# Optimization experiments

Measured on AMD Instinct MI355X. Metric: run time of the kernel, lower is better.

## Reference

```python
import jax, jax.numpy as jnp
import numpy as np

B, L = 2048, 128          # (src,tgt) pairs x walk positions
K = 4                     # num_layers + 1
ENC = 108                 # enc_dim
D2, D3, D4 = 172, 512, 172
NKEYS = 1_000_000         # unique (batch,node,time,sign) keys in nodetime2emb_maps


def setup_inputs() -> dict:
    key = jax.random.key(0)
    ks = jax.random.split(key, 8)
    emb_table = jax.random.uniform(ks[0], (NKEYS, 2, K), dtype=jnp.float32)
    idx = jax.random.randint(ks[1], (B, L), 0, NKEYS, dtype=jnp.int32)
    W1 = jax.random.normal(ks[2], (K, ENC), dtype=jnp.float32) * (1.0 / np.sqrt(K))
    b1 = jnp.zeros((ENC,), dtype=jnp.float32)
    W2 = jax.random.normal(ks[3], (ENC, ENC), dtype=jnp.float32) * (1.0 / np.sqrt(ENC))
    b2 = jnp.zeros((ENC,), dtype=jnp.float32)
    x2 = jax.random.normal(ks[4], (B, L, D2), dtype=jnp.float32)
    fc1_w = jax.random.normal(ks[5], (ENC + D2, D3), dtype=jnp.float32) * (1.0 / np.sqrt(ENC + D2))
    fc1_b = jnp.zeros((D3,), dtype=jnp.float32)
    fc2_w = jax.random.normal(ks[6], (D3, D4), dtype=jnp.float32) * (1.0 / np.sqrt(D3))
    fc2_b = jnp.zeros((D4,), dtype=jnp.float32)
    return {"emb_table": emb_table, "idx": idx, "W1": W1, "b1": b1, "W2": W2,
            "b2": b2, "x2": x2, "fc1_w": fc1_w, "fc1_b": fc1_b,
            "fc2_w": fc2_w, "fc2_b": fc2_b}


def reference(emb_table, idx, W1, b1, W2, b2, x2, fc1_w, fc1_b, fc2_w, fc2_b):
    # --- PositionEncoder.forward: gather per-(node,time) encodings [B,L,2,K]
    enc = emb_table[idx]
    # --- get_trainable_encodings: Linear(K->ENC), ReLU, Linear(ENC->ENC), sum over src/tgt axis
    h = jax.nn.relu(jnp.einsum('blsk,ke->blse', enc, W1) + b1)
    h = jnp.einsum('blse,ef->blsf', h, W2) + b2
    pe = h.sum(axis=-2)                      # [B, L, ENC]
    # --- MergeLayer (edge_embedding_type='concat'): concat + fc1 + ReLU + fc2
    x = jnp.concatenate([pe, x2], axis=-1)   # [B, L, ENC + D2]
    z = jax.nn.relu(x @ fc1_w + fc1_b) @ fc2_w + fc2_b  # [B, L, D4]
    return z
```

## Files before the change

### kernel.cpp

```cpp
#include <hip/hip_runtime.h>
#include <stdint.h>

typedef __bf16 bf16x8 __attribute__((ext_vector_type(8)));
typedef float  f32x4  __attribute__((ext_vector_type(4)));
typedef unsigned short u16x4 __attribute__((ext_vector_type(4)));

#define XROW_B 576
#define HROW_B 1024
#define LDS_SZ 65536
#define WSTG   40960

#define WS_FC1T   0
#define WS_FC2T   294912
#define WS_BIAS   491520

__device__ __forceinline__ unsigned short f2bf(float f) {
  union { float f; unsigned u; } c; c.f = f;
  unsigned u = c.u;
  u += 0x7FFFu + ((u >> 16) & 1u);
  return (unsigned short)(u >> 16);
}

__global__ void POLAR_prep_fc1(const float* __restrict__ W2,
                               const float* __restrict__ fc1_w,
                               const float* __restrict__ fc1_b,
                               const float* __restrict__ b2,
                               unsigned short* __restrict__ fc1t,
                               float* __restrict__ bias_eff) {
  int n = blockIdx.x;
  int k = threadIdx.x;
  float v = 0.f;
  if (k < 108) {
    for (int f = 0; f < 108; ++f) v += W2[k*108 + f] * fc1_w[f*512 + n];
  } else if (k < 280) {
    v = fc1_w[k*512 + n];
  }
  fc1t[n*288 + k] = f2bf(v);
  if (k == 0) {
    float bb = fc1_b[n];
    for (int f = 0; f < 108; ++f) bb += 2.f * b2[f] * fc1_w[f*512 + n];
    bias_eff[n] = bb;
  }
}

__global__ void POLAR_prep_fc2(const float* __restrict__ fc2_w,
                               unsigned short* __restrict__ fc2t) {
  int n = blockIdx.x;
  int k = threadIdx.x;
  float v = (n < 172) ? fc2_w[k*172 + n] : 0.f;
  fc2t[n*512 + k] = f2bf(v);
}

__global__ __launch_bounds__(512, 4) void POLAR_fused(
    const float* __restrict__ emb, const int* __restrict__ idx,
    const float* __restrict__ W1, const float* __restrict__ b1,
    const float* __restrict__ x2,
    const unsigned short* __restrict__ fc1t,
    const float* __restrict__ bias_eff,
    const unsigned short* __restrict__ fc2t,
    const float* __restrict__ fc2b,
    float* __restrict__ out)
{
  __shared__ __attribute__((aligned(16))) char smem[LDS_SZ];
  const int tid  = threadIdx.x;
  const int lane = tid & 63;
  const int w    = tid >> 6;
  const int blk  = blockIdx.x;
  const int l15  = lane & 15;
  const int l4   = lane >> 4;

  const char* fb1 = (const char*)fc1t;
  const char* fb2 = (const char*)fc2t;

  unsigned boff1[4];
  bf16x8 bva[4], bvb[4];
  #pragma unroll
  for (int j = 0; j < 4; ++j) {
    boff1[j] = (unsigned)((w * 64 + j * 16 + l15) * 576 + l4 * 16);
    bva[j] = *(const bf16x8*)(fb1 + boff1[j]);
  }

  const int r  = tid >> 3;
  const int li = tid & 7;
  int key = idx[(size_t)blk * 64 + r];
  const float* ep = emb + (size_t)key * 8;
  f32x4 e0 = *(const f32x4*)ep;
  f32x4 e1 = *(const f32x4*)(ep + 4);

  {
    float* wsl = (float*)(smem + WSTG);
    if (tid < 432) wsl[tid] = W1[tid];
    else if (tid < 540) wsl[tid] = b1[tid - 432];
    int t2 = tid + 512;
    if (t2 < 540) wsl[t2] = b1[t2 - 432];
  }
  __syncthreads();

  {
    const float* Ws = (const float*)(smem + WSTG);
    unsigned sw = ((unsigned)(r >> 1) & 3u) << 4;
    for (int e = li; e < 108; e += 8) {
      float w0 = Ws[e], w1v = Ws[108 + e], w2v = Ws[216 + e], w3v = Ws[324 + e];
      float bb = Ws[432 + e];
      float a0 = fmaxf(e0.x*w0 + e0.y*w1v + e0.z*w2v + e0.w*w3v + bb, 0.f);
      float a1 = fmaxf(e1.x*w0 + e1.y*w1v + e1.z*w2v + e1.w*w3v + bb, 0.f);
      *(unsigned short*)(smem + r * XROW_B + ((unsigned)(2*e) ^ sw)) = f2bf(a0 + a1);
    }
  }

  {
    const f32x4* x2v = (const f32x4*)(x2 + (size_t)blk * 64 * 172);
    #pragma unroll 1
    for (int t = tid; t < 64 * 43; t += 512) {
      int rr = t / 43, c4 = t - rr * 43;
      f32x4 v = x2v[t];
      u16x4 s; s.x = f2bf(v.x); s.y = f2bf(v.y); s.z = f2bf(v.z); s.w = f2bf(v.w);
      unsigned be = 216u + 8u * (unsigned)c4;
      unsigned sw = ((unsigned)(rr >> 1) & 3u) << 4;
      *(u16x4*)(smem + rr * XROW_B + (be ^ sw)) = s;
    }
    if (tid < 64) {
      unsigned sw = ((unsigned)(tid >> 1) & 3u) << 4;
      union { long2 l; } z; z.l.x = 0; z.l.y = 0;
      *(long2*)(smem + tid * XROW_B + (560u ^ sw)) = z.l;
    }
  }
  __syncthreads();

  f32x4 acc[4][4];
  #pragma unroll
  for (int i = 0; i < 4; ++i)
    #pragma unroll
    for (int j = 0; j < 4; ++j)
      acc[i][j] = (f32x4){0.f, 0.f, 0.f, 0.f};

  unsigned abase[4];
  #pragma unroll
  for (int i = 0; i < 4; ++i) {
    int row = i * 16 + l15;
    abase[i] = (unsigned)(row * XROW_B)
             + (((unsigned)(l4 * 16)) ^ ((((unsigned)row >> 1) & 3u) << 4));
  }

  bf16x8 af[4];
  #pragma unroll 1
  for (int kt = 0; kt < 8; kt += 2) {
    #pragma unroll
    for (int j = 0; j < 4; ++j)
      bvb[j] = *(const bf16x8*)(fb1 + boff1[j] + (kt + 1) * 64);
    #pragma unroll
    for (int i = 0; i < 4; ++i)
      af[i] = *(const bf16x8*)(smem + abase[i] + kt * 64);
    #pragma unroll
    for (int i = 0; i < 4; ++i)
      #pragma unroll
      for (int j = 0; j < 4; ++j)
        acc[i][j] = __builtin_amdgcn_mfma_f32_16x16x32_bf16(af[i], bva[j], acc[i][j], 0, 0, 0);
    #pragma unroll
    for (int j = 0; j < 4; ++j)
      bva[j] = *(const bf16x8*)(fb1 + boff1[j] + (kt + 2) * 64);
    #pragma unroll
    for (int i = 0; i < 4; ++i)
      af[i] = *(const bf16x8*)(smem + abase[i] + (kt + 1) * 64);
    #pragma unroll
    for (int i = 0; i < 4; ++i)
      #pragma unroll
      for (int j = 0; j < 4; ++j)
        acc[i][j] = __builtin_amdgcn_mfma_f32_16x16x32_bf16(af[i], bvb[j], acc[i][j], 0, 0, 0);
  }
  {
    #pragma unroll
    for (int i = 0; i < 4; ++i)
      af[i] = *(const bf16x8*)(smem + abase[i] + 8 * 64);
    #pragma unroll
    for (int i = 0; i < 4; ++i)
      #pragma unroll
      for (int j = 0; j < 4; ++j)
        acc[i][j] = __builtin_amdgcn_mfma_f32_16x16x32_bf16(af[i], bva[j], acc[i][j], 0, 0, 0);
  }
  __syncthreads();

  const int wm4 = w >> 2;
  const int wn4 = w & 3;
  unsigned boff2[3];
  bf16x8 b2a[3][2], b2b[3][2];
  #pragma unroll
  for (int j = 0; j < 3; ++j) {
    boff2[j] = (unsigned)((wn4 * 48 + j * 16 + l15) * 1024 + l4 * 16);
    #pragma unroll
    for (int s = 0; s < 2; ++s)
      b2a[j][s] = *(const bf16x8*)(fb2 + boff2[j] + s * 64);
  }

  {
    const int odd = lane & 1;
    #pragma unroll
    for (int i = 0; i < 4; ++i) {
      #pragma unroll
      for (int j = 0; j < 4; ++j) {
        int col0 = w * 64 + j * 16 + l15;
        float be = bias_eff[col0];
        float a0 = fmaxf(acc[i][j][0] + be, 0.f);
        float a1 = fmaxf(acc[i][j][1] + be, 0.f);
        float a2 = fmaxf(acc[i][j][2] + be, 0.f);
        float a3 = fmaxf(acc[i][j][3] + be, 0.f);
        float t0 = odd ? a0 : a2;
        float t1 = odd ? a1 : a3;
        float p0 = __shfl_xor(t0, 1);
        float p1 = __shfl_xor(t1, 1);
        unsigned w0 = odd ? ((unsigned)f2bf(p0) | ((unsigned)f2bf(a2) << 16))
                          : ((unsigned)f2bf(a0) | ((unsigned)f2bf(p0) << 16));
        unsigned w1 = odd ? ((unsigned)f2bf(p1) | ((unsigned)f2bf(a3) << 16))
                          : ((unsigned)f2bf(a1) | ((unsigned)f2bf(p1) << 16));
        int row0 = i * 16 + l4 * 4 + (odd ? 2 : 0);
        int row1 = row0 + 1;
        unsigned cb = (unsigned)((col0 & ~1) * 2);
        *(unsigned*)(smem + row0 * HROW_B + (cb ^ (((unsigned)row0 & 7u) << 4))) = w0;
        *(unsigned*)(smem + row1 * HROW_B + (cb ^ (((unsigned)row1 & 7u) << 4))) = w1;
      }
    }
  }
  __syncthreads();

  f32x4 acc2[2][3];
  #pragma unroll
  for (int i = 0; i < 2; ++i)
    #pragma unroll
    for (int j = 0; j < 3; ++j)
      acc2[i][j] = (f32x4){0.f, 0.f, 0.f, 0.f};

  unsigned h0base[2], swr2[2];
  #pragma unroll
  for (int i = 0; i < 2; ++i) {
    int row = wm4 * 32 + i * 16 + l15;
    h0base[i] = (unsigned)(row * HROW_B);
    swr2[i] = (((unsigned)row & 7u) << 4);
  }

  bf16x8 a2[2][2];
  #pragma unroll 1
  for (int kt = 0; kt < 8; kt += 2) {
    #pragma unroll
    for (int j = 0; j < 3; ++j)
      #pragma unroll
      for (int s = 0; s < 2; ++s)
        b2b[j][s] = *(const bf16x8*)(fb2 + boff2[j] + (kt + 1) * 128 + s * 64);
    #pragma unroll
    for (int i = 0; i < 2; ++i)
      #pragma unroll
      for (int s = 0; s < 2; ++s)
        a2[i][s] = *(const bf16x8*)(smem + h0base[i]
                     + (((unsigned)(kt * 128 + s * 64 + l4 * 16)) ^ swr2[i]));
    #pragma unroll
    for (int s = 0; s < 2; ++s)
      #pragma unroll
      for (int i = 0; i < 2; ++i)
        #pragma unroll
        for (int j = 0; j < 3; ++j)
          acc2[i][j] = __builtin_amdgcn_mfma_f32_16x16x32_bf16(a2[i][s], b2a[j][s], acc2[i][j], 0, 0, 0);
    if (kt < 6) {
      #pragma unroll
      for (int j = 0; j < 3; ++j)
        #pragma unroll
        for (int s = 0; s < 2; ++s)
          b2a[j][s] = *(const bf16x8*)(fb2 + boff2[j] + (kt + 2) * 128 + s * 64);
    }
    #pragma unroll
    for (int i = 0; i < 2; ++i)
      #pragma unroll
      for (int s = 0; s < 2; ++s)
        a2[i][s] = *(const bf16x8*)(smem + h0base[i]
                     + (((unsigned)((kt + 1) * 128 + s * 64 + l4 * 16)) ^ swr2[i]));
    #pragma unroll
    for (int s = 0; s < 2; ++s)
      #pragma unroll
      for (int i = 0; i < 2; ++i)
        #pragma unroll
        for (int j = 0; j < 3; ++j)
          acc2[i][j] = __builtin_amdgcn_mfma_f32_16x16x32_bf16(a2[i][s], b2b[j][s], acc2[i][j], 0, 0, 0);
  }

  const size_t orow0 = (size_t)blk * 64;
  #pragma unroll
  for (int j = 0; j < 3; ++j) {
    int col = wn4 * 48 + j * 16 + l15;
    if (col < 172) {
      float bias = fc2b[col];
      #pragma unroll
      for (int i = 0; i < 2; ++i) {
        #pragma unroll
        for (int r2 = 0; r2 < 4; ++r2) {
          int row = wm4 * 32 + i * 16 + l4 * 4 + r2;
          out[(orow0 + row) * 172 + col] = acc2[i][j][r2] + bias;
        }
      }
    }
  }
}

extern "C" void kernel_launch(void* const* d_in, const int* in_sizes, int n_in,
                              void* d_out, int out_size, void* d_ws, size_t ws_size,
                              hipStream_t stream) {
  (void)in_sizes; (void)n_in; (void)out_size; (void)ws_size;
  const float* emb   = (const float*)d_in[0];
  const int*   idx   = (const int*)d_in[1];
  const float* W1    = (const float*)d_in[2];
  const float* b1    = (const float*)d_in[3];
  const float* W2    = (const float*)d_in[4];
  const float* b2    = (const float*)d_in[5];
  const float* x2    = (const float*)d_in[6];
  const float* fc1_w = (const float*)d_in[7];
  const float* fc1_b = (const float*)d_in[8];
  const float* fc2_w = (const float*)d_in[9];
  const float* fc2_b = (const float*)d_in[10];
  float* out = (float*)d_out;
  char* ws = (char*)d_ws;
  unsigned short* fc1t = (unsigned short*)(ws + WS_FC1T);
  unsigned short* fc2t = (unsigned short*)(ws + WS_FC2T);
  float* bias_eff = (float*)(ws + WS_BIAS);

  POLAR_prep_fc1<<<512, 288, 0, stream>>>(W2, fc1_w, fc1_b, b2, fc1t, bias_eff);
  POLAR_prep_fc2<<<192, 512, 0, stream>>>(fc2_w, fc2t);
  POLAR_fused<<<4096, 512, 0, stream>>>(emb, idx, W1, b1, x2, fc1t, bias_eff,
                                        fc2t, fc2_b, out);
}
```

Measured before the change: 350.2 us.

## Split row preparation into separate kernel and stream bf16 rows via global_load_lds

The gather, first-layer encoding and x2 bf16 conversion move out of the fused GEMM kernel into a new row-prep kernel. It writes swizzled bf16 rows to a workspace buffer, and the GEMM kernel copies them into LDS with global_load_lds DMA. The GEMM kernel's launch bounds change from 4 to 2 blocks per CU. This is meant to take the latency-bound gather and conversion off the MFMA kernel, at the cost of an extra write and read of about 150 MB of bf16 data. The old fused kernel stays as a fallback when the workspace is too small.

```diff
diff --git a/kernel.cpp b/kernel.cpp
--- a/kernel.cpp
+++ b/kernel.cpp
@@ -8,17 +8,24 @@
 #define XROW_B 576
 #define HROW_B 1024
 #define LDS_SZ 65536
-#define WSTG   40960
 
 #define WS_FC1T   0
 #define WS_FC2T   294912
 #define WS_BIAS   491520
+#define WS_XBF    524288
+#define WS_NEED   (524288 + (size_t)262144 * 576)
 
 __device__ __forceinline__ unsigned short f2bf(float f) {
   union { float f; unsigned u; } c; c.f = f;
   unsigned u = c.u;
   u += 0x7FFFu + ((u >> 16) & 1u);
   return (unsigned short)(u >> 16);
+}
+
+__device__ __forceinline__ void g2l16(const void* g, void* l) {
+  __builtin_amdgcn_global_load_lds(
+      (const __attribute__((address_space(1))) void*)g,
+      (__attribute__((address_space(3))) void*)l, 16, 0, 0);
 }
 
 __global__ void POLAR_prep_fc1(const float* __restrict__ W2,
@@ -51,10 +58,63 @@
   fc2t[n*512 + k] = f2bf(v);
 }
 
-__global__ __launch_bounds__(512, 4) void POLAR_fused(
+__global__ __launch_bounds__(256) void POLAR_rows(
     const float* __restrict__ emb, const int* __restrict__ idx,
     const float* __restrict__ W1, const float* __restrict__ b1,
-    const float* __restrict__ x2,
+    const float* __restrict__ x2, unsigned short* __restrict__ xbf)
+{
+  __shared__ float wsl[540];
+  const int tid = threadIdx.x, blk = blockIdx.x;
+
+  const int p = tid >> 1, q = tid & 1;
+  const size_t row = (size_t)blk * 128 + p;
+  int key = idx[row];
+  const float* ep = emb + (size_t)key * 8;
+  f32x4 e0 = *(const f32x4*)ep;
+  f32x4 e1 = *(const f32x4*)(ep + 4);
+
+  for (int t = tid; t < 540; t += 256) wsl[t] = (t < 432) ? W1[t] : b1[t - 432];
+  __syncthreads();
+
+  {
+    char* xrow = (char*)xbf + row * XROW_B;
+    unsigned sw = ((unsigned)(p >> 1) & 3u) << 4;
+    int ebase = q * 54;
+    #pragma unroll 3
+    for (int i = 0; i < 27; ++i) {
+      int e = ebase + 2 * i;
+      float wa0 = wsl[e],     wa1 = wsl[108+e],   wa2 = wsl[216+e],   wa3 = wsl[324+e],   ba = wsl[432+e];
+      float wb0 = wsl[e+1],   wb1 = wsl[109+e],   wb2 = wsl[217+e],   wb3 = wsl[325+e],   bb = wsl[433+e];
+      float a = fmaxf(e0.x*wa0 + e0.y*wa1 + e0.z*wa2 + e0.w*wa3 + ba, 0.f)
+              + fmaxf(e1.x*wa0 + e1.y*wa1 + e1.z*wa2 + e1.w*wa3 + ba, 0.f);
+      float b = fmaxf(e0.x*wb0 + e0.y*wb1 + e0.z*wb2 + e0.w*wb3 + bb, 0.f)
+              + fmaxf(e1.x*wb0 + e1.y*wb1 + e1.z*wb2 + e1.w*wb3 + bb, 0.f);
+      unsigned pk = (unsigned)f2bf(a) | ((unsigned)f2bf(b) << 16);
+      *(unsigned*)(xrow + ((unsigned)(2 * e) ^ sw)) = pk;
+    }
+  }
+
+  {
+    const f32x4* x2v = (const f32x4*)(x2 + (size_t)blk * 128 * 172);
+    char* xbase = (char*)xbf + (size_t)blk * 128 * XROW_B;
+    #pragma unroll 2
+    for (int t = tid; t < 128 * 43; t += 256) {
+      int rr = t / 43, c4 = t - rr * 43;
+      f32x4 v = x2v[t];
+      u16x4 s; s.x = f2bf(v.x); s.y = f2bf(v.y); s.z = f2bf(v.z); s.w = f2bf(v.w);
+      unsigned sw = ((unsigned)(rr >> 1) & 3u) << 4;
+      *(u16x4*)(xbase + rr * XROW_B + ((216u + 8u * (unsigned)c4) ^ sw)) = s;
+    }
+    if (tid < 128) {
+      unsigned sw = ((unsigned)(tid >> 1) & 3u) << 4;
+      union { long2 l; } z; z.l.x = 0; z.l.y = 0;
+      *(long2*)(xbase + tid * XROW_B + (560u ^ sw)) = z.l;
+    }
+  }
+}
+
+__global__ __launch_bounds__(512, 2) void POLAR_gemm(
+    const unsigned short* __restrict__ xbf,
     const unsigned short* __restrict__ fc1t,
     const float* __restrict__ bias_eff,
     const unsigned short* __restrict__ fc2t,
@@ -80,50 +140,11 @@
     bva[j] = *(const bf16x8*)(fb1 + boff1[j]);
   }
 
-  const int r  = tid >> 3;
-  const int li = tid & 7;
-  int key = idx[(size_t)blk * 64 + r];
-  const float* ep = emb + (size_t)key * 8;
-  f32x4 e0 = *(const f32x4*)ep;
-  f32x4 e1 = *(const f32x4*)(ep + 4);
-
-  {
-    float* wsl = (float*)(smem + WSTG);
-    if (tid < 432) wsl[tid] = W1[tid];
-    else if (tid < 540) wsl[tid] = b1[tid - 432];
-    int t2 = tid + 512;
-    if (t2 < 540) wsl[t2] = b1[t2 - 432];
-  }
-  __syncthreads();
-
-  {
-    const float* Ws = (const float*)(smem + WSTG);
-    unsigned sw = ((unsigned)(r >> 1) & 3u) << 4;
-    for (int e = li; e < 108; e += 8) {
-      float w0 = Ws[e], w1v = Ws[108 + e], w2v = Ws[216 + e], w3v = Ws[324 + e];
-      float bb = Ws[432 + e];
-      float a0 = fmaxf(e0.x*w0 + e0.y*w1v + e0.z*w2v + e0.w*w3v + bb, 0.f);
-      float a1 = fmaxf(e1.x*w0 + e1.y*w1v + e1.z*w2v + e1.w*w3v + bb, 0.f);
-      *(unsigned short*)(smem + r * XROW_B + ((unsigned)(2*e) ^ sw)) = f2bf(a0 + a1);
-    }
-  }
-
-  {
-    const f32x4* x2v = (const f32x4*)(x2 + (size_t)blk * 64 * 172);
-    #pragma unroll 1
-    for (int t = tid; t < 64 * 43; t += 512) {
-      int rr = t / 43, c4 = t - rr * 43;
-      f32x4 v = x2v[t];
-      u16x4 s; s.x = f2bf(v.x); s.y = f2bf(v.y); s.z = f2bf(v.z); s.w = f2bf(v.w);
-      unsigned be = 216u + 8u * (unsigned)c4;
-      unsigned sw = ((unsigned)(rr >> 1) & 3u) << 4;
-      *(u16x4*)(smem + rr * XROW_B + (be ^ sw)) = s;
-    }
-    if (tid < 64) {
-      unsigned sw = ((unsigned)(tid >> 1) & 3u) << 4;
-      union { long2 l; } z; z.l.x = 0; z.l.y = 0;
-      *(long2*)(smem + tid * XROW_B + (560u ^ sw)) = z.l;
-    }
+  {
+    const char* xsrc = (const char*)xbf + (size_t)blk * (64 * XROW_B);
+    #pragma unroll
+    for (int c = w; c < 36; c += 8)
+      g2l16(xsrc + c * 1024 + lane * 16, smem + c * 1024);
   }
   __syncthreads();
 
@@ -298,10 +319,256 @@
   }
 }
 
+__global__ __launch_bounds__(512, 4) void POLAR_fused_fb(
+    const float* __restrict__ emb, const int* __restrict__ idx,
+    const float* __restrict__ W1, const float* __restrict__ b1,
+    const float* __restrict__ x2,
+    const unsigned short* __restrict__ fc1t,
+    const float* __restrict__ bias_eff,
+    const unsigned short* __restrict__ fc2t,
+    const float* __restrict__ fc2b,
+    float* __restrict__ out)
+{
+  __shared__ __attribute__((aligned(16))) char smem[LDS_SZ];
+  const int tid  = threadIdx.x;
+  const int lane = tid & 63;
+  const int w    = tid >> 6;
+  const int blk  = blockIdx.x;
+  const int l15  = lane & 15;
+  const int l4   = lane >> 4;
+
+  const char* fb1 = (const char*)fc1t;
+  const char* fb2 = (const char*)fc2t;
+
+  unsigned boff1[4];
+  bf16x8 bva[4], bvb[4];
+  #pragma unroll
+  for (int j = 0; j < 4; ++j) {
+    boff1[j] = (unsigned)((w * 64 + j * 16 + l15) * 576 + l4 * 16);
+    bva[j] = *(const bf16x8*)(fb1 + boff1[j]);
+  }
+
+  const int r  = tid >> 3;
+  const int li = tid & 7;
+  int key = idx[(size_t)blk * 64 + r];
+  const float* ep = emb + (size_t)key * 8;
+  f32x4 e0 = *(const f32x4*)ep;
+  f32x4 e1 = *(const f32x4*)(ep + 4);
+
+  {
+    float* wsl = (float*)(smem + 40960);
+    if (tid < 432) wsl[tid] = W1[tid];
+    else if (tid < 540) wsl[tid] = b1[tid - 432];
+    int t2 = tid + 512;
+    if (t2 < 540) wsl[t2] = b1[t2 - 432];
+  }
+  __syncthreads();
+
+  {
+    const float* Ws = (const float*)(smem + 40960);
+    unsigned sw = ((unsigned)(r >> 1) & 3u) << 4;
+    for (int e = li; e < 108; e += 8) {
+      float w0 = Ws[e], w1v = Ws[108 + e], w2v = Ws[216 + e], w3v = Ws[324 + e];
+      float bb = Ws[432 + e];
+      float a0 = fmaxf(e0.x*w0 + e0.y*w1v + e0.z*w2v + e0.w*w3v + bb, 0.f);
+      float a1 = fmaxf(e1.x*w0 + e1.y*w1v + e1.z*w2v + e1.w*w3v + bb, 0.f);
+      *(unsigned short*)(smem + r * XROW_B + ((unsigned)(2*e) ^ sw)) = f2bf(a0 + a1);
+    }
+  }
+  {
+    const f32x4* x2v = (const f32x4*)(x2 + (size_t)blk * 64 * 172);
+    #pragma unroll 1
+    for (int t = tid; t < 64 * 43; t += 512) {
+      int rr = t / 43, c4 = t - rr * 43;
+      f32x4 v = x2v[t];
+      u16x4 s; s.x = f2bf(v.x); s.y = f2bf(v.y); s.z = f2bf(v.z); s.w = f2bf(v.w);
+      unsigned be = 216u + 8u * (unsigned)c4;
+      unsigned sw = ((unsigned)(rr >> 1) & 3u) << 4;
+      *(u16x4*)(smem + rr * XROW_B + (be ^ sw)) = s;
+    }
+    if (tid < 64) {
+      unsigned sw = ((unsigned)(tid >> 1) & 3u) << 4;
+      union { long2 l; } z; z.l.x = 0; z.l.y = 0;
+      *(long2*)(smem + tid * XROW_B + (560u ^ sw)) = z.l;
+    }
+  }
+  __syncthreads();
+
+  f32x4 acc[4][4];
+  #pragma unroll
+  for (int i = 0; i < 4; ++i)
+    #pragma unroll
+    for (int j = 0; j < 4; ++j)
+      acc[i][j] = (f32x4){0.f, 0.f, 0.f, 0.f};
+
+  unsigned abase[4];
+  #pragma unroll
+  for (int i = 0; i < 4; ++i) {
+    int row = i * 16 + l15;
+    abase[i] = (unsigned)(row * XROW_B)
+             + (((unsigned)(l4 * 16)) ^ ((((unsigned)row >> 1) & 3u) << 4));
+  }
+
+  bf16x8 af[4];
+  #pragma unroll 1
+  for (int kt = 0; kt < 8; kt += 2) {
+    #pragma unroll
+    for (int j = 0; j < 4; ++j)
+      bvb[j] = *(const bf16x8*)(fb1 + boff1[j] + (kt + 1) * 64);
+    #pragma unroll
+    for (int i = 0; i < 4; ++i)
+      af[i] = *(const bf16x8*)(smem + abase[i] + kt * 64);
+    #pragma unroll
+    for (int i = 0; i < 4; ++i)
+      #pragma unroll
+      for (int j = 0; j < 4; ++j)
+        acc[i][j] = __builtin_amdgcn_mfma_f32_16x16x32_bf16(af[i], bva[j], acc[i][j], 0, 0, 0);
+    #pragma unroll
+    for (int j = 0; j < 4; ++j)
+      bva[j] = *(const bf16x8*)(fb1 + boff1[j] + (kt + 2) * 64);
+    #pragma unroll
+    for (int i = 0; i < 4; ++i)
+      af[i] = *(const bf16x8*)(smem + abase[i] + (kt + 1) * 64);
+    #pragma unroll
+    for (int i = 0; i < 4; ++i)
+      #pragma unroll
+      for (int j = 0; j < 4; ++j)
+        acc[i][j] = __builtin_amdgcn_mfma_f32_16x16x32_bf16(af[i], bvb[j], acc[i][j], 0, 0, 0);
+  }
+  {
+    #pragma unroll
+    for (int i = 0; i < 4; ++i)
+      af[i] = *(const bf16x8*)(smem + abase[i] + 8 * 64);
+    #pragma unroll
+    for (int i = 0; i < 4; ++i)
+      #pragma unroll
+      for (int j = 0; j < 4; ++j)
+        acc[i][j] = __builtin_amdgcn_mfma_f32_16x16x32_bf16(af[i], bva[j], acc[i][j], 0, 0, 0);
+  }
+  __syncthreads();
+
+  const int wm4 = w >> 2;
+  const int wn4 = w & 3;
+  unsigned boff2[3];
+  bf16x8 b2a[3][2], b2b[3][2];
+  #pragma unroll
+  for (int j = 0; j < 3; ++j) {
+    boff2[j] = (unsigned)((wn4 * 48 + j * 16 + l15) * 1024 + l4 * 16);
+    #pragma unroll
+    for (int s = 0; s < 2; ++s)
+      b2a[j][s] = *(const bf16x8*)(fb2 + boff2[j] + s * 64);
+  }
+
+  {
+    const int odd = lane & 1;
+    #pragma unroll
+    for (int i = 0; i < 4; ++i) {
+      #pragma unroll
+      for (int j = 0; j < 4; ++j) {
+        int col0 = w * 64 + j * 16 + l15;
+        float be = bias_eff[col0];
+        float a0 = fmaxf(acc[i][j][0] + be, 0.f);
+        float a1 = fmaxf(acc[i][j][1] + be, 0.f);
+        float a2 = fmaxf(acc[i][j][2] + be, 0.f);
+        float a3 = fmaxf(acc[i][j][3] + be, 0.f);
+        float t0 = odd ? a0 : a2;
+        float t1 = odd ? a1 : a3;
+        float p0 = __shfl_xor(t0, 1);
+        float p1 = __shfl_xor(t1, 1);
+        unsigned w0 = odd ? ((unsigned)f2bf(p0) | ((unsigned)f2bf(a2) << 16))
+                          : ((unsigned)f2bf(a0) | ((unsigned)f2bf(p0) << 16));
+        unsigned w1 = odd ? ((unsigned)f2bf(p1) | ((unsigned)f2bf(a3) << 16))
+                          : ((unsigned)f2bf(a1) | ((unsigned)f2bf(p1) << 16));
+        int row0 = i * 16 + l4 * 4 + (odd ? 2 : 0);
+        int row1 = row0 + 1;
+        unsigned cb = (unsigned)((col0 & ~1) * 2);
+        *(unsigned*)(smem + row0 * HROW_B + (cb ^ (((unsigned)row0 & 7u) << 4))) = w0;
+        *(unsigned*)(smem + row1 * HROW_B + (cb ^ (((unsigned)row1 & 7u) << 4))) = w1;
+      }
+    }
+  }
+  __syncthreads();
+
+  f32x4 acc2[2][3];
+  #pragma unroll
+  for (int i = 0; i < 2; ++i)
+    #pragma unroll
+    for (int j = 0; j < 3; ++j)
+      acc2[i][j] = (f32x4){0.f, 0.f, 0.f, 0.f};
+
+  unsigned h0base[2], swr2[2];
+  #pragma unroll
+  for (int i = 0; i < 2; ++i) {
+    int row = wm4 * 32 + i * 16 + l15;
+    h0base[i] = (unsigned)(row * HROW_B);
+    swr2[i] = (((unsigned)row & 7u) << 4);
+  }
+
+  bf16x8 a2[2][2];
+  #pragma unroll 1
+  for (int kt = 0; kt < 8; kt += 2) {
+    #pragma unroll
+    for (int j = 0; j < 3; ++j)
+      #pragma unroll
+      for (int s = 0; s < 2; ++s)
+        b2b[j][s] = *(const bf16x8*)(fb2 + boff2[j] + (kt + 1) * 128 + s * 64);
+    #pragma unroll
+    for (int i = 0; i < 2; ++i)
+      #pragma unroll
+      for (int s = 0; s < 2; ++s)
+        a2[i][s] = *(const bf16x8*)(smem + h0base[i]
+                     + (((unsigned)(kt * 128 + s * 64 + l4 * 16)) ^ swr2[i]));
+    #pragma unroll
+    for (int s = 0; s < 2; ++s)
+      #pragma unroll
+      for (int i = 0; i < 2; ++i)
+        #pragma unroll
+        for (int j = 0; j < 3; ++j)
+          acc2[i][j] = __builtin_amdgcn_mfma_f32_16x16x32_bf16(a2[i][s], b2a[j][s], acc2[i][j], 0, 0, 0);
+    if (kt < 6) {
+      #pragma unroll
+      for (int j = 0; j < 3; ++j)
+        #pragma unroll
+        for (int s = 0; s < 2; ++s)
+          b2a[j][s] = *(const bf16x8*)(fb2 + boff2[j] + (kt + 2) * 128 + s * 64);
+    }
+    #pragma unroll
+    for (int i = 0; i < 2; ++i)
+      #pragma unroll
+      for (int s = 0; s < 2; ++s)
+        a2[i][s] = *(const bf16x8*)(smem + h0base[i]
+                     + (((unsigned)((kt + 1) * 128 + s * 64 + l4 * 16)) ^ swr2[i]));
+    #pragma unroll
+    for (int s = 0; s < 2; ++s)
+      #pragma unroll
+      for (int i = 0; i < 2; ++i)
+        #pragma unroll
+        for (int j = 0; j < 3; ++j)
+          acc2[i][j] = __builtin_amdgcn_mfma_f32_16x16x32_bf16(a2[i][s], b2b[j][s], acc2[i][j], 0, 0, 0);
+  }
+
+  const size_t orow0 = (size_t)blk * 64;
+  #pragma unroll
+  for (int j = 0; j < 3; ++j) {
+    int col = wn4 * 48 + j * 16 + l15;
+    if (col < 172) {
+      float bias = fc2b[col];
+      #pragma unroll
+      for (int i = 0; i < 2; ++i) {
+        #pragma unroll
+        for (int r2 = 0; r2 < 4; ++r2) {
+          int row = wm4 * 32 + i * 16 + l4 * 4 + r2;
+          out[(orow0 + row) * 172 + col] = acc2[i][j][r2] + bias;
+        }
+      }
+    }
+  }
+}
+
 extern "C" void kernel_launch(void* const* d_in, const int* in_sizes, int n_in,
                               void* d_out, int out_size, void* d_ws, size_t ws_size,
                               hipStream_t stream) {
-  (void)in_sizes; (void)n_in; (void)out_size; (void)ws_size;
+  (void)in_sizes; (void)n_in; (void)out_size;
   const float* emb   = (const float*)d_in[0];
   const int*   idx   = (const int*)d_in[1];
   const float* W1    = (const float*)d_in[2];
@@ -321,6 +588,13 @@
 
   POLAR_prep_fc1<<<512, 288, 0, stream>>>(W2, fc1_w, fc1_b, b2, fc1t, bias_eff);
   POLAR_prep_fc2<<<192, 512, 0, stream>>>(fc2_w, fc2t);
-  POLAR_fused<<<4096, 512, 0, stream>>>(emb, idx, W1, b1, x2, fc1t, bias_eff,
-                                        fc2t, fc2_b, out);
-}
+
+  if (ws_size >= WS_NEED) {
+    unsigned short* xbf = (unsigned short*)(ws + WS_XBF);
+    POLAR_rows<<<2048, 256, 0, stream>>>(emb, idx, W1, b1, x2, xbf);
+    POLAR_gemm<<<4096, 512, 0, stream>>>(xbf, fc1t, bias_eff, fc2t, fc2_b, out);
+  } else {
+    POLAR_fused_fb<<<4096, 512, 0, stream>>>(emb, idx, W1, b1, x2, fc1t, bias_eff,
+                                             fc2t, fc2_b, out);
+  }
+}
```

Result: slower. 462.1 us (+31.9%).

## Split row prep into separate kernel and pipeline persistent GEMM over tiles

Applied to the files above, without the earlier changes.

Moves the embedding gather, first-layer encoding and x2 bf16 conversion into a separate kernel that writes a pre-swizzled bf16 activation buffer to workspace. The GEMM kernel then runs persistently over 8 tiles per block. It loads each tile into LDS with direct global-to-LDS copies, and half the waves prefetch the next tile while the other half write the hidden activations. The hidden buffer is halved and fc2 is done in two K-halves to free LDS for this overlap. The cost is an extra global round trip of the bf16 activations, about 300MB of write plus read, and more barriers per tile.

```diff
diff --git a/kernel.cpp b/kernel.cpp
--- a/kernel.cpp
+++ b/kernel.cpp
@@ -6,19 +6,30 @@
 typedef unsigned short u16x4 __attribute__((ext_vector_type(4)));
 
 #define XROW_B 576
-#define HROW_B 1024
-#define LDS_SZ 65536
-#define WSTG   40960
+#define HROW_B 512
+#define X_OFF  0
+#define H_OFF  36864
+#define LDS_G  69632
+
+#define RLDS_W  73728
+#define RLDS_SZ 75904
 
 #define WS_FC1T   0
 #define WS_FC2T   294912
 #define WS_BIAS   491520
+#define WS_XBF    524288
 
 __device__ __forceinline__ unsigned short f2bf(float f) {
   union { float f; unsigned u; } c; c.f = f;
   unsigned u = c.u;
   u += 0x7FFFu + ((u >> 16) & 1u);
   return (unsigned short)(u >> 16);
+}
+
+__device__ __forceinline__ void g2l16(const void* g, void* l) {
+  __builtin_amdgcn_global_load_lds(
+      (const __attribute__((address_space(1))) void*)g,
+      (__attribute__((address_space(3))) void*)l, 16, 0, 0);
 }
 
 __global__ void POLAR_prep_fc1(const float* __restrict__ W2,
@@ -51,89 +62,89 @@
   fc2t[n*512 + k] = f2bf(v);
 }
 
-__global__ __launch_bounds__(512, 4) void POLAR_fused(
+__global__ __launch_bounds__(512) void POLAR_rows(
     const float* __restrict__ emb, const int* __restrict__ idx,
     const float* __restrict__ W1, const float* __restrict__ b1,
-    const float* __restrict__ x2,
+    const float* __restrict__ x2, unsigned short* __restrict__ xbf)
+{
+  __shared__ __attribute__((aligned(16))) char rsm[RLDS_SZ];
+  const int tid = threadIdx.x, blk = blockIdx.x;
+
+  const int p = tid >> 2, q = tid & 3;
+  const size_t row = (size_t)blk * 128 + p;
+  int key = idx[row];
+  const float* ep = emb + (size_t)key * 8;
+  f32x4 e0 = *(const f32x4*)ep;
+  f32x4 e1 = *(const f32x4*)(ep + 4);
+
+  float* wsl = (float*)(rsm + RLDS_W);
+  for (int tt = tid; tt < 540; tt += 512)
+    wsl[tt] = (tt < 432) ? W1[tt] : b1[tt - 432];
+  __syncthreads();
+
+  {
+    unsigned sw = ((unsigned)(p >> 1) & 3u) << 4;
+    char* xr = rsm + p * XROW_B;
+    int eb = q * 27;
+    #pragma unroll 1
+    for (int i2 = 0; i2 < 27; ++i2) {
+      int e = eb + i2;
+      float w0 = wsl[e], w1v = wsl[108+e], w2v = wsl[216+e], w3v = wsl[324+e];
+      float bb = wsl[432+e];
+      float a0 = fmaxf(e0.x*w0 + e0.y*w1v + e0.z*w2v + e0.w*w3v + bb, 0.f);
+      float a1 = fmaxf(e1.x*w0 + e1.y*w1v + e1.z*w2v + e1.w*w3v + bb, 0.f);
+      *(unsigned short*)(xr + ((unsigned)(2*e) ^ sw)) = f2bf(a0 + a1);
+    }
+  }
+
+  {
+    const f32x4* x2v = (const f32x4*)(x2 + (size_t)blk * 128 * 172);
+    #pragma unroll 1
+    for (int tt = tid; tt < 128 * 43; tt += 512) {
+      int rr = tt / 43, c4 = tt - rr * 43;
+      f32x4 v = x2v[tt];
+      u16x4 s; s.x = f2bf(v.x); s.y = f2bf(v.y); s.z = f2bf(v.z); s.w = f2bf(v.w);
+      unsigned sw = ((unsigned)(rr >> 1) & 3u) << 4;
+      *(u16x4*)(rsm + rr * XROW_B + ((216u + 8u * (unsigned)c4) ^ sw)) = s;
+    }
+    if (tid < 128) {
+      unsigned sw = ((unsigned)(tid >> 1) & 3u) << 4;
+      f32x4 z = (f32x4){0.f, 0.f, 0.f, 0.f};
+      *(f32x4*)(rsm + tid * XROW_B + (560u ^ sw)) = z;
+    }
+  }
+  __syncthreads();
+
+  {
+    f32x4* dst = (f32x4*)((char*)xbf + (size_t)blk * 73728);
+    const f32x4* src = (const f32x4*)rsm;
+    #pragma unroll
+    for (int k2 = 0; k2 < 9; ++k2)
+      dst[tid + k2 * 512] = src[tid + k2 * 512];
+  }
+}
+
+__global__ __launch_bounds__(512, 4) void POLAR_gemm(
+    const unsigned short* __restrict__ xbf,
     const unsigned short* __restrict__ fc1t,
     const float* __restrict__ bias_eff,
     const unsigned short* __restrict__ fc2t,
     const float* __restrict__ fc2b,
     float* __restrict__ out)
 {
-  __shared__ __attribute__((aligned(16))) char smem[LDS_SZ];
+  __shared__ __attribute__((aligned(16))) char smem[LDS_G];
   const int tid  = threadIdx.x;
   const int lane = tid & 63;
   const int w    = tid >> 6;
-  const int blk  = blockIdx.x;
   const int l15  = lane & 15;
   const int l4   = lane >> 4;
-
   const char* fb1 = (const char*)fc1t;
   const char* fb2 = (const char*)fc2t;
 
   unsigned boff1[4];
-  bf16x8 bva[4], bvb[4];
-  #pragma unroll
-  for (int j = 0; j < 4; ++j) {
+  #pragma unroll
+  for (int j = 0; j < 4; ++j)
     boff1[j] = (unsigned)((w * 64 + j * 16 + l15) * 576 + l4 * 16);
-    bva[j] = *(const bf16x8*)(fb1 + boff1[j]);
-  }
-
-  const int r  = tid >> 3;
-  const int li = tid & 7;
-  int key = idx[(size_t)blk * 64 + r];
-  const float* ep = emb + (size_t)key * 8;
-  f32x4 e0 = *(const f32x4*)ep;
-  f32x4 e1 = *(const f32x4*)(ep + 4);
-
-  {
-    float* wsl = (float*)(smem + WSTG);
-    if (tid < 432) wsl[tid] = W1[tid];
-    else if (tid < 540) wsl[tid] = b1[tid - 432];
-    int t2 = tid + 512;
-    if (t2 < 540) wsl[t2] = b1[t2 - 432];
-  }
-  __syncthreads();
-
-  {
-    const float* Ws = (const float*)(smem + WSTG);
-    unsigned sw = ((unsigned)(r >> 1) & 3u) << 4;
-    for (int e = li; e < 108; e += 8) {
-      float w0 = Ws[e], w1v = Ws[108 + e], w2v = Ws[216 + e], w3v = Ws[324 + e];
-      float bb = Ws[432 + e];
-      float a0 = fmaxf(e0.x*w0 + e0.y*w1v + e0.z*w2v + e0.w*w3v + bb, 0.f);
-      float a1 = fmaxf(e1.x*w0 + e1.y*w1v + e1.z*w2v + e1.w*w3v + bb, 0.f);
-      *(unsigned short*)(smem + r * XROW_B + ((unsigned)(2*e) ^ sw)) = f2bf(a0 + a1);
-    }
-  }
-
-  {
-    const f32x4* x2v = (const f32x4*)(x2 + (size_t)blk * 64 * 172);
-    #pragma unroll 1
-    for (int t = tid; t < 64 * 43; t += 512) {
-      int rr = t / 43, c4 = t - rr * 43;
-      f32x4 v = x2v[t];
-      u16x4 s; s.x = f2bf(v.x); s.y = f2bf(v.y); s.z = f2bf(v.z); s.w = f2bf(v.w);
-      unsigned be = 216u + 8u * (unsigned)c4;
-      unsigned sw = ((unsigned)(rr >> 1) & 3u) << 4;
-      *(u16x4*)(smem + rr * XROW_B + (be ^ sw)) = s;
-    }
-    if (tid < 64) {
-      unsigned sw = ((unsigned)(tid >> 1) & 3u) << 4;
-      union { long2 l; } z; z.l.x = 0; z.l.y = 0;
-      *(long2*)(smem + tid * XROW_B + (560u ^ sw)) = z.l;
-    }
-  }
-  __syncthreads();
-
-  f32x4 acc[4][4];
-  #pragma unroll
-  for (int i = 0; i < 4; ++i)
-    #pragma unroll
-    for (int j = 0; j < 4; ++j)
-      acc[i][j] = (f32x4){0.f, 0.f, 0.f, 0.f};
-
   unsigned abase[4];
   #pragma unroll
   for (int i = 0; i < 4; ++i) {
@@ -141,157 +152,234 @@
     abase[i] = (unsigned)(row * XROW_B)
              + (((unsigned)(l4 * 16)) ^ ((((unsigned)row >> 1) & 3u) << 4));
   }
-
-  bf16x8 af[4];
-  #pragma unroll 1
-  for (int kt = 0; kt < 8; kt += 2) {
-    #pragma unroll
-    for (int j = 0; j < 4; ++j)
-      bvb[j] = *(const bf16x8*)(fb1 + boff1[j] + (kt + 1) * 64);
-    #pragma unroll
-    for (int i = 0; i < 4; ++i)
-      af[i] = *(const bf16x8*)(smem + abase[i] + kt * 64);
-    #pragma unroll
-    for (int i = 0; i < 4; ++i)
-      #pragma unroll
-      for (int j = 0; j < 4; ++j)
-        acc[i][j] = __builtin_amdgcn_mfma_f32_16x16x32_bf16(af[i], bva[j], acc[i][j], 0, 0, 0);
-    #pragma unroll
-    for (int j = 0; j < 4; ++j)
-      bva[j] = *(const bf16x8*)(fb1 + boff1[j] + (kt + 2) * 64);
-    #pragma unroll
-    for (int i = 0; i < 4; ++i)
-      af[i] = *(const bf16x8*)(smem + abase[i] + (kt + 1) * 64);
-    #pragma unroll
-    for (int i = 0; i < 4; ++i)
-      #pragma unroll
-      for (int j = 0; j < 4; ++j)
-        acc[i][j] = __builtin_amdgcn_mfma_f32_16x16x32_bf16(af[i], bvb[j], acc[i][j], 0, 0, 0);
-  }
-  {
-    #pragma unroll
-    for (int i = 0; i < 4; ++i)
-      af[i] = *(const bf16x8*)(smem + abase[i] + 8 * 64);
-    #pragma unroll
-    for (int i = 0; i < 4; ++i)
-      #pragma unroll
-      for (int j = 0; j < 4; ++j)
-        acc[i][j] = __builtin_amdgcn_mfma_f32_16x16x32_bf16(af[i], bva[j], acc[i][j], 0, 0, 0);
-  }
-  __syncthreads();
-
-  const int wm4 = w >> 2;
-  const int wn4 = w & 3;
+  const int wm4 = w >> 2, wn4 = w & 3;
   unsigned boff2[3];
-  bf16x8 b2a[3][2], b2b[3][2];
-  #pragma unroll
-  for (int j = 0; j < 3; ++j) {
+  #pragma unroll
+  for (int j = 0; j < 3; ++j)
     boff2[j] = (unsigned)((wn4 * 48 + j * 16 + l15) * 1024 + l4 * 16);
-    #pragma unroll
-    for (int s = 0; s < 2; ++s)
-      b2a[j][s] = *(const bf16x8*)(fb2 + boff2[j] + s * 64);
-  }
-
-  {
-    const int odd = lane & 1;
-    #pragma unroll
-    for (int i = 0; i < 4; ++i) {
-      #pragma unroll
-      for (int j = 0; j < 4; ++j) {
-        int col0 = w * 64 + j * 16 + l15;
-        float be = bias_eff[col0];
-        float a0 = fmaxf(acc[i][j][0] + be, 0.f);
-        float a1 = fmaxf(acc[i][j][1] + be, 0.f);
-        float a2 = fmaxf(acc[i][j][2] + be, 0.f);
-        float a3 = fmaxf(acc[i][j][3] + be, 0.f);
-        float t0 = odd ? a0 : a2;
-        float t1 = odd ? a1 : a3;
-        float p0 = __shfl_xor(t0, 1);
-        float p1 = __shfl_xor(t1, 1);
-        unsigned w0 = odd ? ((unsigned)f2bf(p0) | ((unsigned)f2bf(a2) << 16))
-                          : ((unsigned)f2bf(a0) | ((unsigned)f2bf(p0) << 16));
-        unsigned w1 = odd ? ((unsigned)f2bf(p1) | ((unsigned)f2bf(a3) << 16))
-                          : ((unsigned)f2bf(a1) | ((unsigned)f2bf(p1) << 16));
-        int row0 = i * 16 + l4 * 4 + (odd ? 2 : 0);
-        int row1 = row0 + 1;
-        unsigned cb = (unsigned)((col0 & ~1) * 2);
-        *(unsigned*)(smem + row0 * HROW_B + (cb ^ (((unsigned)row0 & 7u) << 4))) = w0;
-        *(unsigned*)(smem + row1 * HROW_B + (cb ^ (((unsigned)row1 & 7u) << 4))) = w1;
-      }
-    }
-  }
-  __syncthreads();
-
-  f32x4 acc2[2][3];
-  #pragma unroll
-  for (int i = 0; i < 2; ++i)
-    #pragma unroll
-    for (int j = 0; j < 3; ++j)
-      acc2[i][j] = (f32x4){0.f, 0.f, 0.f, 0.f};
-
-  unsigned h0base[2], swr2[2];
+  unsigned h2base[2], swr2[2];
   #pragma unroll
   for (int i = 0; i < 2; ++i) {
     int row = wm4 * 32 + i * 16 + l15;
-    h0base[i] = (unsigned)(row * HROW_B);
+    h2base[i] = (unsigned)(H_OFF + row * HROW_B);
     swr2[i] = (((unsigned)row & 7u) << 4);
   }
 
-  bf16x8 a2[2][2];
+  const size_t tile0 = (size_t)blockIdx.x * 8;
+  {
+    const char* xsrc = (const char*)xbf + tile0 * 36864;
+    for (int c = w; c < 36; c += 8)
+      g2l16(xsrc + c * 1024 + lane * 16, smem + X_OFF + c * 1024);
+  }
+  bf16x8 bva[4], bvb[4];
+  #pragma unroll
+  for (int j = 0; j < 4; ++j) bva[j] = *(const bf16x8*)(fb1 + boff1[j]);
+  bf16x8 b2c[3][2];
+  #pragma unroll
+  for (int j = 0; j < 3; ++j)
+    #pragma unroll
+    for (int s = 0; s < 2; ++s)
+      b2c[j][s] = *(const bf16x8*)(fb2 + boff2[j] + s * 64);
+
   #pragma unroll 1
-  for (int kt = 0; kt < 8; kt += 2) {
-    #pragma unroll
-    for (int j = 0; j < 3; ++j)
+  for (int t = 0; t < 8; ++t) {
+    const size_t tile = tile0 + t;
+    __syncthreads();
+
+    f32x4 acc[4][4];
+    #pragma unroll
+    for (int i = 0; i < 4; ++i)
+      #pragma unroll
+      for (int j = 0; j < 4; ++j)
+        acc[i][j] = (f32x4){0.f, 0.f, 0.f, 0.f};
+
+    bf16x8 af[4];
+    #pragma unroll 1
+    for (int kt = 0; kt < 8; kt += 2) {
+      #pragma unroll
+      for (int j = 0; j < 4; ++j)
+        bvb[j] = *(const bf16x8*)(fb1 + boff1[j] + (kt + 1) * 64);
+      #pragma unroll
+      for (int i = 0; i < 4; ++i)
+        af[i] = *(const bf16x8*)(smem + X_OFF + abase[i] + kt * 64);
+      #pragma unroll
+      for (int i = 0; i < 4; ++i)
+        #pragma unroll
+        for (int j = 0; j < 4; ++j)
+          acc[i][j] = __builtin_amdgcn_mfma_f32_16x16x32_bf16(af[i], bva[j], acc[i][j], 0, 0, 0);
+      #pragma unroll
+      for (int j = 0; j < 4; ++j)
+        bva[j] = *(const bf16x8*)(fb1 + boff1[j] + (kt + 2) * 64);
+      #pragma unroll
+      for (int i = 0; i < 4; ++i)
+        af[i] = *(const bf16x8*)(smem + X_OFF + abase[i] + (kt + 1) * 64);
+      #pragma unroll
+      for (int i = 0; i < 4; ++i)
+        #pragma unroll
+        for (int j = 0; j < 4; ++j)
+          acc[i][j] = __builtin_amdgcn_mfma_f32_16x16x32_bf16(af[i], bvb[j], acc[i][j], 0, 0, 0);
+    }
+    {
+      #pragma unroll
+      for (int i = 0; i < 4; ++i)
+        af[i] = *(const bf16x8*)(smem + X_OFF + abase[i] + 8 * 64);
+      #pragma unroll
+      for (int i = 0; i < 4; ++i)
+        #pragma unroll
+        for (int j = 0; j < 4; ++j)
+          acc[i][j] = __builtin_amdgcn_mfma_f32_16x16x32_bf16(af[i], bva[j], acc[i][j], 0, 0, 0);
+    }
+    #pragma unroll
+    for (int j = 0; j < 4; ++j) bva[j] = *(const bf16x8*)(fb1 + boff1[j]);
+
+    __syncthreads();
+
+    if (w >= 4) {
+      if (t < 7) {
+        const char* xsrc = (const char*)xbf + (tile + 1) * 36864;
+        for (int c = (w - 4); c < 36; c += 4)
+          g2l16(xsrc + c * 1024 + lane * 16, smem + X_OFF + c * 1024);
+      }
+    } else {
+      const int odd = lane & 1;
+      #pragma unroll
+      for (int i = 0; i < 4; ++i) {
+        #pragma unroll
+        for (int j = 0; j < 4; ++j) {
+          int col0 = w * 64 + j * 16 + l15;
+          float be = bias_eff[col0];
+          float a0 = fmaxf(acc[i][j][0] + be, 0.f);
+          float a1 = fmaxf(acc[i][j][1] + be, 0.f);
+          float a2 = fmaxf(acc[i][j][2] + be, 0.f);
+          float a3 = fmaxf(acc[i][j][3] + be, 0.f);
+          float t0 = odd ? a0 : a2;
+          float t1 = odd ? a1 : a3;
+          float p0 = __shfl_xor(t0, 1);
+          float p1 = __shfl_xor(t1, 1);
+          unsigned w0 = odd ? ((unsigned)f2bf(p0) | ((unsigned)f2bf(a2) << 16))
+                            : ((unsigned)f2bf(a0) | ((unsigned)f2bf(p0) << 16));
+          unsigned w1 = odd ? ((unsigned)f2bf(p1) | ((unsigned)f2bf(a3) << 16))
+                            : ((unsigned)f2bf(a1) | ((unsigned)f2bf(p1) << 16));
+          int row0 = i * 16 + l4 * 4 + (odd ? 2 : 0);
+          int row1 = row0 + 1;
+          unsigned cb = (unsigned)((col0 & ~1) * 2);
+          *(unsigned*)(smem + H_OFF + row0 * HROW_B + (cb ^ (((unsigned)row0 & 7u) << 4))) = w0;
+          *(unsigned*)(smem + H_OFF + row1 * HROW_B + (cb ^ (((unsigned)row1 & 7u) << 4))) = w1;
+        }
+      }
+    }
+    __syncthreads();
+
+    f32x4 acc2[2][3];
+    #pragma unroll
+    for (int i = 0; i < 2; ++i)
+      #pragma unroll
+      for (int j = 0; j < 3; ++j)
+        acc2[i][j] = (f32x4){0.f, 0.f, 0.f, 0.f};
+
+    #pragma unroll
+    for (int kt = 0; kt < 4; ++kt) {
+      bf16x8 b2n[3][2];
+      #pragma unroll
+      for (int j = 0; j < 3; ++j)
+        #pragma unroll
+        for (int s = 0; s < 2; ++s)
+          b2n[j][s] = *(const bf16x8*)(fb2 + boff2[j] + (kt + 1) * 128 + s * 64);
+      bf16x8 a2v[2][2];
+      #pragma unroll
+      for (int i = 0; i < 2; ++i)
+        #pragma unroll
+        for (int s = 0; s < 2; ++s)
+          a2v[i][s] = *(const bf16x8*)(smem + h2base[i]
+                       + (((unsigned)(kt * 128 + s * 64 + l4 * 16)) ^ swr2[i]));
       #pragma unroll
       for (int s = 0; s < 2; ++s)
-        b2b[j][s] = *(const bf16x8*)(fb2 + boff2[j] + (kt + 1) * 128 + s * 64);
-    #pragma unroll
-    for (int i = 0; i < 2; ++i)
+        #pragma unroll
+        for (int i = 0; i < 2; ++i)
+          #pragma unroll
+          for (int j = 0; j < 3; ++j)
+            acc2[i][j] = __builtin_amdgcn_mfma_f32_16x16x32_bf16(a2v[i][s], b2c[j][s], acc2[i][j], 0, 0, 0);
+      #pragma unroll
+      for (int j = 0; j < 3; ++j)
+        #pragma unroll
+        for (int s = 0; s < 2; ++s)
+          b2c[j][s] = b2n[j][s];
+    }
+    __syncthreads();
+
+    if (w >= 4) {
+      const int odd = lane & 1;
+      #pragma unroll
+      for (int i = 0; i < 4; ++i) {
+        #pragma unroll
+        for (int j = 0; j < 4; ++j) {
+          int col0 = w * 64 + j * 16 + l15;
+          float be = bias_eff[col0];
+          float a0 = fmaxf(acc[i][j][0] + be, 0.f);
+          float a1 = fmaxf(acc[i][j][1] + be, 0.f);
+          float a2 = fmaxf(acc[i][j][2] + be, 0.f);
+          float a3 = fmaxf(acc[i][j][3] + be, 0.f);
+          float t0 = odd ? a0 : a2;
+          float t1 = odd ? a1 : a3;
+          float p0 = __shfl_xor(t0, 1);
+          float p1 = __shfl_xor(t1, 1);
+          unsigned w0 = odd ? ((unsigned)f2bf(p0) | ((unsigned)f2bf(a2) << 16))
+                            : ((unsigned)f2bf(a0) | ((unsigned)f2bf(p0) << 16));
+          unsigned w1 = odd ? ((unsigned)f2bf(p1) | ((unsigned)f2bf(a3) << 16))
+                            : ((unsigned)f2bf(a1) | ((unsigned)f2bf(p1) << 16));
+          int row0 = i * 16 + l4 * 4 + (odd ? 2 : 0);
+          int row1 = row0 + 1;
+          unsigned cb = (unsigned)(((col0 - 256) & ~1) * 2);
+          *(unsigned*)(smem + H_OFF + row0 * HROW_B + (cb ^ (((unsigned)row0 & 7u) << 4))) = w0;
+          *(unsigned*)(smem + H_OFF + row1 * HROW_B + (cb ^ (((unsigned)row1 & 7u) << 4))) = w1;
+        }
+      }
+    }
+    __syncthreads();
+
+    #pragma unroll
+    for (int kt = 4; kt < 8; ++kt) {
+      bf16x8 b2n[3][2];
+      #pragma unroll
+      for (int j = 0; j < 3; ++j)
+        #pragma unroll
+        for (int s = 0; s < 2; ++s)
+          b2n[j][s] = *(const bf16x8*)(fb2 + boff2[j]
+                        + ((kt + 1 < 8) ? (kt + 1) * 128 : 0) + s * 64);
+      bf16x8 a2v[2][2];
+      #pragma unroll
+      for (int i = 0; i < 2; ++i)
+        #pragma unroll
+        for (int s = 0; s < 2; ++s)
+          a2v[i][s] = *(const bf16x8*)(smem + h2base[i]
+                       + (((unsigned)((kt - 4) * 128 + s * 64 + l4 * 16)) ^ swr2[i]));
       #pragma unroll
       for (int s = 0; s < 2; ++s)
-        a2[i][s] = *(const bf16x8*)(smem + h0base[i]
-                     + (((unsigned)(kt * 128 + s * 64 + l4 * 16)) ^ swr2[i]));
-    #pragma unroll
-    for (int s = 0; s < 2; ++s)
-      #pragma unroll
-      for (int i = 0; i < 2; ++i)
-        #pragma unroll
-        for (int j = 0; j < 3; ++j)
-          acc2[i][j] = __builtin_amdgcn_mfma_f32_16x16x32_bf16(a2[i][s], b2a[j][s], acc2[i][j], 0, 0, 0);
-    if (kt < 6) {
+        #pragma unroll
+        for (int i = 0; i < 2; ++i)
+          #pragma unroll
+          for (int j = 0; j < 3; ++j)
+            acc2[i][j] = __builtin_amdgcn_mfma_f32_16x16x32_bf16(a2v[i][s], b2c[j][s], acc2[i][j], 0, 0, 0);
       #pragma unroll
       for (int j = 0; j < 3; ++j)
         #pragma unroll
         for (int s = 0; s < 2; ++s)
-          b2a[j][s] = *(const bf16x8*)(fb2 + boff2[j] + (kt + 2) * 128 + s * 64);
-    }
-    #pragma unroll
-    for (int i = 0; i < 2; ++i)
-      #pragma unroll
-      for (int s = 0; s < 2; ++s)
-        a2[i][s] = *(const bf16x8*)(smem + h0base[i]
-                     + (((unsigned)((kt + 1) * 128 + s * 64 + l4 * 16)) ^ swr2[i]));
-    #pragma unroll
-    for (int s = 0; s < 2; ++s)
-      #pragma unroll
-      for (int i = 0; i < 2; ++i)
-        #pragma unroll
-        for (int j = 0; j < 3; ++j)
-          acc2[i][j] = __builtin_amdgcn_mfma_f32_16x16x32_bf16(a2[i][s], b2b[j][s], acc2[i][j], 0, 0, 0);
-  }
-
-  const size_t orow0 = (size_t)blk * 64;
-  #pragma unroll
-  for (int j = 0; j < 3; ++j) {
-    int col = wn4 * 48 + j * 16 + l15;
-    if (col < 172) {
-      float bias = fc2b[col];
-      #pragma unroll
-      for (int i = 0; i < 2; ++i) {
-        #pragma unroll
-        for (int r2 = 0; r2 < 4; ++r2) {
-          int row = wm4 * 32 + i * 16 + l4 * 4 + r2;
-          out[(orow0 + row) * 172 + col] = acc2[i][j][r2] + bias;
+          b2c[j][s] = b2n[j][s];
+    }
+
+    const size_t orow0 = tile * 64;
+    #pragma unroll
+    for (int j = 0; j < 3; ++j) {
+      int col = wn4 * 48 + j * 16 + l15;
+      if (col < 172) {
+        float bias = fc2b[col];
+        #pragma unroll
+        for (int i = 0; i < 2; ++i) {
+          #pragma unroll
+          for (int r2 = 0; r2 < 4; ++r2) {
+            int row = wm4 * 32 + i * 16 + l4 * 4 + r2;
+            out[(orow0 + row) * 172 + col] = acc2[i][j][r2] + bias;
+          }
         }
       }
     }
@@ -318,9 +406,10 @@
   unsigned short* fc1t = (unsigned short*)(ws + WS_FC1T);
   unsigned short* fc2t = (unsigned short*)(ws + WS_FC2T);
   float* bias_eff = (float*)(ws + WS_BIAS);
+  unsigned short* xbf  = (unsigned short*)(ws + WS_XBF);
 
   POLAR_prep_fc1<<<512, 288, 0, stream>>>(W2, fc1_w, fc1_b, b2, fc1t, bias_eff);
   POLAR_prep_fc2<<<192, 512, 0, stream>>>(fc2_w, fc2t);
-  POLAR_fused<<<4096, 512, 0, stream>>>(emb, idx, W1, b1, x2, fc1t, bias_eff,
-                                        fc2t, fc2_b, out);
-}
+  POLAR_rows<<<2048, 512, 0, stream>>>(emb, idx, W1, b1, x2, xbf);
+  POLAR_gemm<<<512, 512, 0, stream>>>(xbf, fc1t, bias_eff, fc2t, fc2_b, out);
+}
```

Result: slower. 810.4 us (+131.4%).
